# Kernel tuning notes

Measured on AMD Instinct MI355X. Metric: run time of the kernel, lower is better.

Reference implementation:

```python
import jax, jax.numpy as jnp
import numpy as np

EPS = 1e-8  # matches torch cosine_similarity eps


def setup_inputs() -> dict:
    key = jax.random.key(0)
    ks = jax.random.split(key, 8)
    B, D_IN, H, L = 256, 256, 256, 100000
    G = 5 * H  # (N_GATES + 1) * hidden_dim
    s_in = 1.0 / np.sqrt(D_IN)
    s_h = 1.0 / np.sqrt(H)
    return {
        "x_t": jax.random.normal(ks[0], (B, D_IN), jnp.float32),
        "h": jax.random.normal(ks[1], (B, H), jnp.float32),
        "c": jax.random.normal(ks[2], (B, H), jnp.float32),
        "W_i2h": jax.random.normal(ks[3], (G, D_IN), jnp.float32) * s_in,
        "b_i2h": jnp.zeros((G,), jnp.float32),
        "W_h2h": jax.random.normal(ks[4], (G, H), jnp.float32) * s_h,
        "b_h2h": jnp.zeros((G,), jnp.float32),
        "keys": jax.random.normal(ks[5], (L, D_IN), jnp.float32),
        "vals": jax.random.normal(ks[6], (L, H), jnp.float32),
    }


def _dnd_get_memory(q, keys, vals):
    # cosine similarity of each query against every stored key -> [B, L]
    qn = q / jnp.maximum(jnp.linalg.norm(q, axis=-1, keepdims=True), EPS)
    kn = keys / jnp.maximum(jnp.linalg.norm(keys, axis=-1, keepdims=True), EPS)
    sims = jnp.einsum("bd,ld->bl", qn, kn)
    w = jax.nn.softmax(sims, axis=-1)          # softmax-weighted aggregation
    return jnp.einsum("bl,lh->bh", w, vals)    # [B, H]


def reference(x_t, h, c, W_i2h, b_i2h, W_h2h, b_h2h, keys, vals):
    H = h.shape[1]
    preact = (x_t @ W_i2h.T + b_i2h) + (h @ W_h2h.T + b_h2h)   # [B, 5H]
    gates = jax.nn.sigmoid(preact[:, : 4 * H])
    f_t = gates[:, :H]
    i_t = gates[:, H:2 * H]
    o_t = gates[:, 2 * H:3 * H]
    r_t = gates[:, 3 * H:4 * H]
    c_t_new = jnp.tanh(preact[:, 4 * H:])
    c_t = f_t * c + i_t * c_t_new
    m_t = jnp.tanh(_dnd_get_memory(x_t, keys, vals))
    c_t = c_t + r_t * m_t
    h_t = o_t * jnp.tanh(c_t)
    return (h_t, c_t)
```

## Files before the change

### kernel.cpp

```cpp
#include <hip/hip_runtime.h>
#include <stdint.h>

typedef float f4_t __attribute__((ext_vector_type(4)));
typedef __bf16 bf8_t __attribute__((ext_vector_type(8)));
typedef unsigned short us4_t __attribute__((ext_vector_type(4)));
typedef unsigned short us8_t __attribute__((ext_vector_type(8)));

static __device__ __forceinline__ unsigned short f2bf(float f) {
    union { float f; uint32_t u; } v; v.f = f;
    uint32_t r = v.u + 0x7FFFu + ((v.u >> 16) & 1u);
    return (unsigned short)(r >> 16);
}
static __device__ __forceinline__ float bf2f(unsigned short u) {
    union { uint32_t u; float f; } v; v.u = ((uint32_t)u) << 16;
    return v.f;
}
static __device__ __forceinline__ f4_t mfma16(bf8_t a, bf8_t b, f4_t c) {
    return __builtin_amdgcn_mfma_f32_16x16x32_bf16(a, b, c, 0, 0, 0);
}
static __device__ __forceinline__ float sigf(float x) {
    return 1.0f / (1.0f + __expf(-x));
}
static __device__ __forceinline__ void gload_lds16(const void* g, void* l) {
    __builtin_amdgcn_global_load_lds(
        (const __attribute__((address_space(1))) void*)g,
        (__attribute__((address_space(3))) void*)l, 16, 0, 0);
}

__global__ __launch_bounds__(256) void k_convert(
    const float* __restrict__ x, const float* __restrict__ h,
    const float* __restrict__ W1, const float* __restrict__ W2,
    unsigned short* __restrict__ qn, unsigned short* __restrict__ xb,
    unsigned short* __restrict__ hb, unsigned short* __restrict__ w1b,
    unsigned short* __restrict__ w2b)
{
    __shared__ float sred[4];
    int bid = blockIdx.x, t = threadIdx.x;
    if (bid < 256) {
        float v = x[bid * 256 + t];
        float ss = v * v;
        #pragma unroll
        for (int m = 1; m < 64; m <<= 1) ss += __shfl_xor(ss, m, 64);
        if ((t & 63) == 0) sred[t >> 6] = ss;
        __syncthreads();
        float tot = sred[0] + sred[1] + sred[2] + sred[3];
        float rn = 1.0f / fmaxf(sqrtf(tot), 1e-8f);
        xb[bid * 256 + t] = f2bf(v);
        qn[bid * 256 + t] = f2bf(v * rn);
    } else if (bid < 512) {
        int b = bid - 256;
        hb[b * 256 + t] = f2bf(h[b * 256 + t]);
    } else {
        int i0 = (bid - 512) * 256 + t;
        for (int i = i0; i < 1280 * 256; i += 512 * 256) {
            w1b[i] = f2bf(W1[i]);
            w2b[i] = f2bf(W2[i]);
        }
    }
}

__global__ __launch_bounds__(256) void k_gates(
    const unsigned short* __restrict__ xb, const unsigned short* __restrict__ hb,
    const unsigned short* __restrict__ w1b, const unsigned short* __restrict__ w2b,
    const float* __restrict__ b1, const float* __restrict__ b2,
    float* __restrict__ pre)
{
    int bb = (blockIdx.x & 3) * 64;
    int gb = (blockIdx.x >> 2) * 64;
    int t = threadIdx.x, w = t >> 6, lane = t & 63;
    int l15 = lane & 15, q8 = (lane >> 4) * 8, q4 = (lane >> 4) * 4;
    int arow = bb + w * 16 + l15;

    f4_t acc[4] = {};
    #pragma unroll
    for (int ks = 0; ks < 8; ++ks) {
        bf8_t a = *(const bf8_t*)&xb[arow * 256 + ks * 32 + q8];
        #pragma unroll
        for (int gc = 0; gc < 4; ++gc) {
            bf8_t bf = *(const bf8_t*)&w1b[(gb + gc * 16 + l15) * 256 + ks * 32 + q8];
            acc[gc] = mfma16(a, bf, acc[gc]);
        }
    }
    #pragma unroll
    for (int ks = 0; ks < 8; ++ks) {
        bf8_t a = *(const bf8_t*)&hb[arow * 256 + ks * 32 + q8];
        #pragma unroll
        for (int gc = 0; gc < 4; ++gc) {
            bf8_t bf = *(const bf8_t*)&w2b[(gb + gc * 16 + l15) * 256 + ks * 32 + q8];
            acc[gc] = mfma16(a, bf, acc[gc]);
        }
    }
    #pragma unroll
    for (int gc = 0; gc < 4; ++gc) {
        int g = gb + gc * 16 + l15;
        float bias = b1[g] + b2[g];
        #pragma unroll
        for (int r = 0; r < 4; ++r) {
            int b = bb + w * 16 + q4 + r;
            pre[b * 1280 + g] = acc[gc][r] + bias;
        }
    }
}

__global__ __launch_bounds__(256) void k_prep(
    const float* __restrict__ keys, unsigned short* __restrict__ kn, int L)
{
    int tile = blockIdx.x;
    int t = threadIdx.x;
    int w4 = t >> 6;
    int lane = t & 63;
    int c0 = lane * 4;
    #pragma unroll 4
    for (int it = 0; it < 16; ++it) {
        int ri = it * 4 + w4;
        int grow = tile * 64 + ri;
        us4_t uv = {0, 0, 0, 0};
        if (grow < L) {
            f4_t v = *(const f4_t*)&keys[(size_t)grow * 256 + c0];
            float ss = v[0]*v[0] + v[1]*v[1] + v[2]*v[2] + v[3]*v[3];
            #pragma unroll
            for (int m = 1; m < 64; m <<= 1) ss += __shfl_xor(ss, m, 64);
            float rn = 1.0f / fmaxf(sqrtf(ss), 1e-8f);
            uv[0] = f2bf(v[0]*rn); uv[1] = f2bf(v[1]*rn);
            uv[2] = f2bf(v[2]*rn); uv[3] = f2bf(v[3]*rn);
        }
        *(us4_t*)&kn[(size_t)tile * 16384 + ri * 256 + (c0 ^ ((ri & 7) << 3))] = uv;
    }
}

__global__ __launch_bounds__(512, 2) void k_dnd(
    const float* __restrict__ vals, const unsigned short* __restrict__ kn,
    const unsigned short* __restrict__ qn,
    unsigned short* __restrict__ opart, float* __restrict__ dpart,
    int L, int CH, int TILES)
{
    __shared__ __align__(16) char smem[114688];
    unsigned short* Vl = (unsigned short*)(smem + 65536);
    unsigned short* Pl = (unsigned short*)(smem + 98304);

    const int t = threadIdx.x;
    const int w = t >> 6;
    const int lane = t & 63;
    const int l15 = lane & 15;
    const int q8 = (lane >> 4) * 8;
    const int q4 = (lane >> 4) * 4;

    const int bid = blockIdx.x;
    const int bhalf = (bid >> 3) & 1;
    const int chunk = (bid & 7) | ((bid >> 4) << 3);
    const int base = chunk * CH;
    int nkeys = L - base;
    if (nkeys > CH) nkeys = CH;
    if (nkeys < 0) nkeys = 0;
    const int nt = (nkeys + 63) >> 6;

    const int h4 = lane * 4;

    bf8_t qa[8];
    #pragma unroll
    for (int ks = 0; ks < 8; ++ks)
        qa[ks] = *(const bf8_t*)&qn[(bhalf * 128 + w * 16 + l15) * 256 + ks * 32 + q8];

    f4_t o[16] = {};
    float den[4] = {};
    f4_t vst[8];

    if (nt > 0) {
        {
            size_t koff = (size_t)(chunk * TILES) * 32768;
            #pragma unroll
            for (int c = 0; c < 4; ++c)
                gload_lds16((const char*)kn + koff + c * 8192 + w * 1024 + lane * 16,
                            smem + c * 8192 + w * 1024);
            #pragma unroll
            for (int r = 0; r < 8; ++r) {
                int row = base + w * 8 + r;
                row = min(row, L - 1);
                vst[r] = *(const f4_t*)&vals[(size_t)row * 256 + h4];
            }
        }

        for (int tt = 0; tt < nt; ++tt) {
            const int cur = tt & 1;
            {
                int tn = tt + 1 < nt ? tt + 1 : nt - 1;
                size_t koff = (size_t)(chunk * TILES + tn) * 32768;
                char* kb = smem + (cur ^ 1) * 32768;
                #pragma unroll
                for (int c = 0; c < 4; ++c)
                    gload_lds16((const char*)kn + koff + c * 8192 + w * 1024 + lane * 16,
                                kb + c * 8192 + w * 1024);
            }
            asm volatile("s_waitcnt vmcnt(4)" ::: "memory");
            #pragma unroll
            for (int j = 0; j < 4; ++j) {
                int hh = h4 + j;
                us8_t uv;
                #pragma unroll
                for (int r = 0; r < 8; ++r) uv[r] = f2bf(vst[r][j]);
                *(us8_t*)&Vl[hh * 64 + ((w * 8) ^ ((hh & 7) << 3))] = uv;
            }
            {
                int tn = tt + 1 < nt ? tt + 1 : nt - 1;
                #pragma unroll
                for (int r = 0; r < 8; ++r) {
                    int row = base + tn * 64 + w * 8 + r;
                    row = min(row, L - 1);
                    vst[r] = *(const f4_t*)&vals[(size_t)row * 256 + h4];
                }
            }
            asm volatile("s_waitcnt lgkmcnt(0)\n\ts_barrier" ::: "memory");
            __builtin_amdgcn_sched_barrier(0);

            const unsigned short* Kl = (const unsigned short*)(smem + cur * 32768);
            f4_t s[4] = {};
            __builtin_amdgcn_s_setprio(1);
            #pragma unroll
            for (int lc = 0; lc < 4; ++lc) {
                int l = lc * 16 + l15;
                int sw = (l & 7) << 3;
                #pragma unroll
                for (int ks = 0; ks < 8; ++ks) {
                    bf8_t kf = *(const bf8_t*)&Kl[l * 256 + ((ks * 32 + q8) ^ sw)];
                    s[lc] = mfma16(qa[ks], kf, s[lc]);
                }
            }
            __builtin_amdgcn_s_setprio(0);

            #pragma unroll
            for (int lc = 0; lc < 4; ++lc) {
                int l = lc * 16 + l15;
                bool valid = (tt * 64 + l) < nkeys;
                #pragma unroll
                for (int r = 0; r < 4; ++r) {
                    float p = valid ? __expf(s[lc][r] - 1.0f) : 0.0f;
                    den[r] += p;
                    int br = w * 16 + q4 + r;
                    Pl[br * 64 + (l ^ ((br & 7) << 3))] = f2bf(p);
                }
            }

            {
                int brow = w * 16 + l15;
                int swp = (brow & 7) << 3;
                bf8_t pa0 = *(const bf8_t*)&Pl[brow * 64 + (q8 ^ swp)];
                bf8_t pa1 = *(const bf8_t*)&Pl[brow * 64 + ((32 + q8) ^ swp)];
                __builtin_amdgcn_s_setprio(1);
                #pragma unroll
                for (int hc = 0; hc < 16; ++hc) {
                    int hh = hc * 16 + l15;
                    int swv = (hh & 7) << 3;
                    bf8_t vf0 = *(const bf8_t*)&Vl[hh * 64 + (q8 ^ swv)];
                    bf8_t vf1 = *(const bf8_t*)&Vl[hh * 64 + ((32 + q8) ^ swv)];
                    o[hc] = mfma16(pa0, vf0, o[hc]);
                    o[hc] = mfma16(pa1, vf1, o[hc]);
                }
                __builtin_amdgcn_s_setprio(0);
            }

            asm volatile("s_waitcnt lgkmcnt(0)\n\ts_barrier" ::: "memory");
        }
    }

    asm volatile("s_waitcnt vmcnt(0)" ::: "memory");
    __syncthreads();
    unsigned short* Ol = (unsigned short*)smem;
    #pragma unroll
    for (int hc = 0; hc < 16; ++hc)
        #pragma unroll
        for (int r = 0; r < 4; ++r)
            Ol[(w * 16 + q4 + r) * 256 + hc * 16 + l15] = f2bf(o[hc][r]);
    __syncthreads();
    {
        size_t ob = (size_t)(chunk * 2 + bhalf) * 32768;
        #pragma unroll
        for (int it = 0; it < 8; ++it) {
            int off = it * 4096 + t * 8;
            *(us8_t*)&opart[ob + off] = *(const us8_t*)&Ol[off];
        }
    }
    #pragma unroll
    for (int r = 0; r < 4; ++r) {
        float d = den[r];
        #pragma unroll
        for (int m = 1; m < 16; m <<= 1) d += __shfl_xor(d, m, 64);
        if (l15 == 0)
            dpart[chunk * 256 + bhalf * 128 + w * 16 + q4 + r] = d;
    }
}

__global__ __launch_bounds__(256) void k_reduce(
    const unsigned short* __restrict__ opart, const float* __restrict__ dpart,
    const float* __restrict__ pre, const float* __restrict__ c_in,
    float* __restrict__ out)
{
    __shared__ float sred[4];
    int b = blockIdx.x, t = threadIdx.x;

    float ds = (t < 128) ? dpart[t * 256 + b] : 0.0f;
    #pragma unroll
    for (int m = 1; m < 64; m <<= 1) ds += __shfl_xor(ds, m, 64);
    if ((t & 63) == 0) sred[t >> 6] = ds;
    __syncthreads();
    float dtot = fmaxf(sred[0] + sred[1] + sred[2] + sred[3], 1e-30f);

    int bh = b >> 7, br = b & 127;
    float n0 = 0.f, n1 = 0.f, n2 = 0.f, n3 = 0.f;
    for (int ck = 0; ck < 128; ck += 4) {
        n0 += bf2f(opart[(size_t)((ck + 0) * 2 + bh) * 32768 + br * 256 + t]);
        n1 += bf2f(opart[(size_t)((ck + 1) * 2 + bh) * 32768 + br * 256 + t]);
        n2 += bf2f(opart[(size_t)((ck + 2) * 2 + bh) * 32768 + br * 256 + t]);
        n3 += bf2f(opart[(size_t)((ck + 3) * 2 + bh) * 32768 + br * 256 + t]);
    }
    float num = (n0 + n1) + (n2 + n3);

    float m = tanhf(num / dtot);
    const float* p = pre + b * 1280;
    float fg = sigf(p[t]);
    float ig = sigf(p[256 + t]);
    float og = sigf(p[512 + t]);
    float rg = sigf(p[768 + t]);
    float cn = tanhf(p[1024 + t]);
    float co = c_in[b * 256 + t];
    float ct = fg * co + ig * cn + rg * m;
    float ht = og * tanhf(ct);
    out[b * 256 + t] = ht;
    out[65536 + b * 256 + t] = ct;
}

extern "C" void kernel_launch(void* const* d_in, const int* in_sizes, int n_in,
                              void* d_out, int out_size, void* d_ws, size_t ws_size,
                              hipStream_t stream)
{
    const float* x    = (const float*)d_in[0];
    const float* h    = (const float*)d_in[1];
    const float* c    = (const float*)d_in[2];
    const float* W1   = (const float*)d_in[3];
    const float* b1   = (const float*)d_in[4];
    const float* W2   = (const float*)d_in[5];
    const float* b2   = (const float*)d_in[6];
    const float* keys = (const float*)d_in[7];
    const float* vals = (const float*)d_in[8];
    int L = in_sizes[7] / 256;

    int TILES = (L + 128 * 64 - 1) / (128 * 64);
    int CH = TILES * 64;

    char* ws = (char*)d_ws;
    unsigned short* qn    = (unsigned short*)(ws + 0);
    unsigned short* xb    = (unsigned short*)(ws + 131072);
    unsigned short* hb    = (unsigned short*)(ws + 262144);
    unsigned short* w1b   = (unsigned short*)(ws + 393216);
    unsigned short* w2b   = (unsigned short*)(ws + 1048576);
    float*          pre   = (float*)(ws + 1703936);
    float*          dpart = (float*)(ws + 3014656);
    unsigned short* kn    = (unsigned short*)(ws + 3145728);
    unsigned short* opart = (unsigned short*)(ws + 3145728 + (size_t)128 * TILES * 32768);

    k_convert<<<dim3(1024), dim3(256), 0, stream>>>(x, h, W1, W2, qn, xb, hb, w1b, w2b);
    k_gates<<<dim3(80), dim3(256), 0, stream>>>(xb, hb, w1b, w2b, b1, b2, pre);
    k_prep<<<dim3(128 * TILES), dim3(256), 0, stream>>>(keys, kn, L);
    k_dnd<<<dim3(256), dim3(512), 0, stream>>>(vals, kn, qn, opart, dpart, L, CH, TILES);
    k_reduce<<<dim3(256), dim3(256), 0, stream>>>(opart, dpart, pre, c, (float*)d_out);

    (void)n_in; (void)out_size; (void)ws_size;
}
```

Before: 110.5 us.

## Fuse key normalization into DND kernel and drop separate prep pass

Result: slower. 121.4 us (+9.8%).

```diff
diff --git a/kernel.cpp b/kernel.cpp
--- a/kernel.cpp
+++ b/kernel.cpp
@@ -6,10 +6,9 @@
 typedef unsigned short us4_t __attribute__((ext_vector_type(4)));
 typedef unsigned short us8_t __attribute__((ext_vector_type(8)));
 
-static __device__ __forceinline__ unsigned short f2bf(float f) {
-    union { float f; uint32_t u; } v; v.f = f;
-    uint32_t r = v.u + 0x7FFFu + ((v.u >> 16) & 1u);
-    return (unsigned short)(r >> 16);
+static __device__ __forceinline__ unsigned short fbf(float f) {
+    __bf16 b = (__bf16)f;
+    return *(unsigned short*)&b;
 }
 static __device__ __forceinline__ float bf2f(unsigned short u) {
     union { uint32_t u; float f; } v; v.u = ((uint32_t)u) << 16;
@@ -20,11 +19,6 @@
 }
 static __device__ __forceinline__ float sigf(float x) {
     return 1.0f / (1.0f + __expf(-x));
-}
-static __device__ __forceinline__ void gload_lds16(const void* g, void* l) {
-    __builtin_amdgcn_global_load_lds(
-        (const __attribute__((address_space(1))) void*)g,
-        (__attribute__((address_space(3))) void*)l, 16, 0, 0);
 }
 
 __global__ __launch_bounds__(256) void k_convert(
@@ -45,16 +39,16 @@
         __syncthreads();
         float tot = sred[0] + sred[1] + sred[2] + sred[3];
         float rn = 1.0f / fmaxf(sqrtf(tot), 1e-8f);
-        xb[bid * 256 + t] = f2bf(v);
-        qn[bid * 256 + t] = f2bf(v * rn);
+        xb[bid * 256 + t] = fbf(v);
+        qn[bid * 256 + t] = fbf(v * rn);
     } else if (bid < 512) {
         int b = bid - 256;
-        hb[b * 256 + t] = f2bf(h[b * 256 + t]);
+        hb[b * 256 + t] = fbf(h[b * 256 + t]);
     } else {
         int i0 = (bid - 512) * 256 + t;
         for (int i = i0; i < 1280 * 256; i += 512 * 256) {
-            w1b[i] = f2bf(W1[i]);
-            w2b[i] = f2bf(W2[i]);
+            w1b[i] = fbf(W1[i]);
+            w2b[i] = fbf(W2[i]);
         }
     }
 }
@@ -102,41 +96,14 @@
     }
 }
 
-__global__ __launch_bounds__(256) void k_prep(
-    const float* __restrict__ keys, unsigned short* __restrict__ kn, int L)
-{
-    int tile = blockIdx.x;
-    int t = threadIdx.x;
-    int w4 = t >> 6;
-    int lane = t & 63;
-    int c0 = lane * 4;
-    #pragma unroll 4
-    for (int it = 0; it < 16; ++it) {
-        int ri = it * 4 + w4;
-        int grow = tile * 64 + ri;
-        us4_t uv = {0, 0, 0, 0};
-        if (grow < L) {
-            f4_t v = *(const f4_t*)&keys[(size_t)grow * 256 + c0];
-            float ss = v[0]*v[0] + v[1]*v[1] + v[2]*v[2] + v[3]*v[3];
-            #pragma unroll
-            for (int m = 1; m < 64; m <<= 1) ss += __shfl_xor(ss, m, 64);
-            float rn = 1.0f / fmaxf(sqrtf(ss), 1e-8f);
-            uv[0] = f2bf(v[0]*rn); uv[1] = f2bf(v[1]*rn);
-            uv[2] = f2bf(v[2]*rn); uv[3] = f2bf(v[3]*rn);
-        }
-        *(us4_t*)&kn[(size_t)tile * 16384 + ri * 256 + (c0 ^ ((ri & 7) << 3))] = uv;
-    }
-}
-
 __global__ __launch_bounds__(512, 2) void k_dnd(
-    const float* __restrict__ vals, const unsigned short* __restrict__ kn,
+    const float* __restrict__ keys, const float* __restrict__ vals,
     const unsigned short* __restrict__ qn,
     unsigned short* __restrict__ opart, float* __restrict__ dpart,
-    int L, int CH, int TILES)
-{
-    __shared__ __align__(16) char smem[114688];
-    unsigned short* Vl = (unsigned short*)(smem + 65536);
-    unsigned short* Pl = (unsigned short*)(smem + 98304);
+    int L, int CH)
+{
+    __shared__ __align__(16) char smem[147456];
+    unsigned short* Pl = (unsigned short*)(smem + 131072);
 
     const int t = threadIdx.x;
     const int w = t >> 6;
@@ -154,7 +121,10 @@
     if (nkeys < 0) nkeys = 0;
     const int nt = (nkeys + 63) >> 6;
 
-    const int h4 = lane * 4;
+    const int kr = t >> 3;
+    const int kc = (t & 7) * 32;
+    const int vm = t & 63;
+    const int vlw = t >> 6;
 
     bf8_t qa[8];
     #pragma unroll
@@ -163,62 +133,76 @@
 
     f4_t o[16] = {};
     float den[4] = {};
-    f4_t vst[8];
+    f4_t kst[8], vst[8];
+
+    auto issueK = [&](int tt) {
+        int row = base + tt * 64 + kr;
+        row = min(row, L - 1);
+        const float* src = keys + (size_t)row * 256 + kc;
+        #pragma unroll
+        for (int i = 0; i < 8; ++i) kst[i] = *(const f4_t*)(src + 4 * i);
+    };
+    auto issueV = [&](int tt) {
+        #pragma unroll
+        for (int r = 0; r < 8; ++r) {
+            int row = base + tt * 64 + vlw * 8 + r;
+            row = min(row, L - 1);
+            vst[r] = *(const f4_t*)&vals[(size_t)row * 256 + vm * 4];
+        }
+    };
+    auto writeK = [&](char* kb) {
+        float ss = 0.f;
+        #pragma unroll
+        for (int i = 0; i < 8; ++i)
+            ss += kst[i][0]*kst[i][0] + kst[i][1]*kst[i][1]
+                + kst[i][2]*kst[i][2] + kst[i][3]*kst[i][3];
+        ss += __shfl_xor(ss, 1, 64);
+        ss += __shfl_xor(ss, 2, 64);
+        ss += __shfl_xor(ss, 4, 64);
+        float rn = 1.0f / fmaxf(sqrtf(ss), 1e-8f);
+        unsigned short* K = (unsigned short*)kb;
+        #pragma unroll
+        for (int jj = 0; jj < 4; ++jj) {
+            us8_t uv;
+            #pragma unroll
+            for (int d = 0; d < 4; ++d) {
+                uv[d]     = fbf(kst[jj*2][d] * rn);
+                uv[d + 4] = fbf(kst[jj*2 + 1][d] * rn);
+            }
+            *(us8_t*)&K[kr * 256 + ((kc + 8*jj) ^ ((kr & 7) * 8))] = uv;
+        }
+    };
+    auto writeV = [&](char* vb) {
+        unsigned short* V = (unsigned short*)vb;
+        #pragma unroll
+        for (int j = 0; j < 4; ++j) {
+            int hh = vm * 4 + j;
+            int g = (vm ^ (j << 1)) & 7;
+            us8_t uv;
+            #pragma unroll
+            for (int r = 0; r < 8; ++r) uv[r] = fbf(vst[r][j]);
+            *(us8_t*)&V[hh * 64 + ((vlw * 8) ^ (g * 8))] = uv;
+        }
+    };
 
     if (nt > 0) {
-        {
-            size_t koff = (size_t)(chunk * TILES) * 32768;
-            #pragma unroll
-            for (int c = 0; c < 4; ++c)
-                gload_lds16((const char*)kn + koff + c * 8192 + w * 1024 + lane * 16,
-                            smem + c * 8192 + w * 1024);
-            #pragma unroll
-            for (int r = 0; r < 8; ++r) {
-                int row = base + w * 8 + r;
-                row = min(row, L - 1);
-                vst[r] = *(const f4_t*)&vals[(size_t)row * 256 + h4];
-            }
-        }
+        issueK(0); issueV(0);
+        asm volatile("s_waitcnt vmcnt(0)" ::: "memory");
+        writeK(smem); writeV(smem + 65536);
+        if (nt > 1) { issueK(1); issueV(1); }
+        asm volatile("s_waitcnt lgkmcnt(0)\n\ts_barrier" ::: "memory");
 
         for (int tt = 0; tt < nt; ++tt) {
             const int cur = tt & 1;
-            {
-                int tn = tt + 1 < nt ? tt + 1 : nt - 1;
-                size_t koff = (size_t)(chunk * TILES + tn) * 32768;
-                char* kb = smem + (cur ^ 1) * 32768;
-                #pragma unroll
-                for (int c = 0; c < 4; ++c)
-                    gload_lds16((const char*)kn + koff + c * 8192 + w * 1024 + lane * 16,
-                                kb + c * 8192 + w * 1024);
-            }
-            asm volatile("s_waitcnt vmcnt(4)" ::: "memory");
-            #pragma unroll
-            for (int j = 0; j < 4; ++j) {
-                int hh = h4 + j;
-                us8_t uv;
-                #pragma unroll
-                for (int r = 0; r < 8; ++r) uv[r] = f2bf(vst[r][j]);
-                *(us8_t*)&Vl[hh * 64 + ((w * 8) ^ ((hh & 7) << 3))] = uv;
-            }
-            {
-                int tn = tt + 1 < nt ? tt + 1 : nt - 1;
-                #pragma unroll
-                for (int r = 0; r < 8; ++r) {
-                    int row = base + tn * 64 + w * 8 + r;
-                    row = min(row, L - 1);
-                    vst[r] = *(const f4_t*)&vals[(size_t)row * 256 + h4];
-                }
-            }
-            asm volatile("s_waitcnt lgkmcnt(0)\n\ts_barrier" ::: "memory");
-            __builtin_amdgcn_sched_barrier(0);
-
             const unsigned short* Kl = (const unsigned short*)(smem + cur * 32768);
+            const unsigned short* Vl = (const unsigned short*)(smem + 65536 + cur * 32768);
+
             f4_t s[4] = {};
             __builtin_amdgcn_s_setprio(1);
             #pragma unroll
             for (int lc = 0; lc < 4; ++lc) {
                 int l = lc * 16 + l15;
-                int sw = (l & 7) << 3;
+                int sw = (l & 7) * 8;
                 #pragma unroll
                 for (int ks = 0; ks < 8; ++ks) {
                     bf8_t kf = *(const bf8_t*)&Kl[l * 256 + ((ks * 32 + q8) ^ sw)];
@@ -236,40 +220,46 @@
                     float p = valid ? __expf(s[lc][r] - 1.0f) : 0.0f;
                     den[r] += p;
                     int br = w * 16 + q4 + r;
-                    Pl[br * 64 + (l ^ ((br & 7) << 3))] = f2bf(p);
+                    Pl[br * 64 + (l ^ ((br & 7) * 8))] = fbf(p);
                 }
             }
 
             {
                 int brow = w * 16 + l15;
-                int swp = (brow & 7) << 3;
+                int swp = (brow & 7) * 8;
                 bf8_t pa0 = *(const bf8_t*)&Pl[brow * 64 + (q8 ^ swp)];
                 bf8_t pa1 = *(const bf8_t*)&Pl[brow * 64 + ((32 + q8) ^ swp)];
                 __builtin_amdgcn_s_setprio(1);
                 #pragma unroll
                 for (int hc = 0; hc < 16; ++hc) {
                     int hh = hc * 16 + l15;
-                    int swv = (hh & 7) << 3;
-                    bf8_t vf0 = *(const bf8_t*)&Vl[hh * 64 + (q8 ^ swv)];
-                    bf8_t vf1 = *(const bf8_t*)&Vl[hh * 64 + ((32 + q8) ^ swv)];
+                    int g = ((hh >> 2) ^ ((hh & 3) << 1)) & 7;
+                    bf8_t vf0 = *(const bf8_t*)&Vl[hh * 64 + (q8 ^ (g * 8))];
+                    bf8_t vf1 = *(const bf8_t*)&Vl[hh * 64 + ((32 + q8) ^ (g * 8))];
                     o[hc] = mfma16(pa0, vf0, o[hc]);
                     o[hc] = mfma16(pa1, vf1, o[hc]);
                 }
                 __builtin_amdgcn_s_setprio(0);
             }
 
-            asm volatile("s_waitcnt lgkmcnt(0)\n\ts_barrier" ::: "memory");
-        }
-    }
-
-    asm volatile("s_waitcnt vmcnt(0)" ::: "memory");
+            if (tt + 1 < nt) {
+                asm volatile("s_waitcnt vmcnt(0)" ::: "memory");
+                char* kb = smem + (cur ^ 1) * 32768;
+                char* vb = smem + 65536 + (cur ^ 1) * 32768;
+                writeK(kb); writeV(vb);
+                if (tt + 2 < nt) { issueK(tt + 2); issueV(tt + 2); }
+                asm volatile("s_waitcnt lgkmcnt(0)\n\ts_barrier" ::: "memory");
+            }
+        }
+    }
+
     __syncthreads();
     unsigned short* Ol = (unsigned short*)smem;
     #pragma unroll
     for (int hc = 0; hc < 16; ++hc)
         #pragma unroll
         for (int r = 0; r < 4; ++r)
-            Ol[(w * 16 + q4 + r) * 256 + hc * 16 + l15] = f2bf(o[hc][r]);
+            Ol[(w * 16 + q4 + r) * 256 + hc * 16 + l15] = fbf(o[hc][r]);
     __syncthreads();
     {
         size_t ob = (size_t)(chunk * 2 + bhalf) * 32768;
@@ -354,13 +344,11 @@
     unsigned short* w2b   = (unsigned short*)(ws + 1048576);
     float*          pre   = (float*)(ws + 1703936);
     float*          dpart = (float*)(ws + 3014656);
-    unsigned short* kn    = (unsigned short*)(ws + 3145728);
-    unsigned short* opart = (unsigned short*)(ws + 3145728 + (size_t)128 * TILES * 32768);
+    unsigned short* opart = (unsigned short*)(ws + 3145728);
 
     k_convert<<<dim3(1024), dim3(256), 0, stream>>>(x, h, W1, W2, qn, xb, hb, w1b, w2b);
     k_gates<<<dim3(80), dim3(256), 0, stream>>>(xb, hb, w1b, w2b, b1, b2, pre);
-    k_prep<<<dim3(128 * TILES), dim3(256), 0, stream>>>(keys, kn, L);
-    k_dnd<<<dim3(256), dim3(512), 0, stream>>>(vals, kn, qn, opart, dpart, L, CH, TILES);
+    k_dnd<<<dim3(256), dim3(512), 0, stream>>>(keys, vals, qn, opart, dpart, L, CH);
     k_reduce<<<dim3(256), dim3(256), 0, stream>>>(opart, dpart, pre, c, (float*)d_out);
 
     (void)n_in; (void)out_size; (void)ws_size;
```
